# Optimization experiments

Measured on AMD Instinct MI355X. Metric: run time of the kernel, lower is better.

## Reference

```python
import jax, jax.numpy as jnp
import numpy as np

BS, C_IN, S1 = 64, 256, 32
D_OUT, J = 32, 10          # out_dim, num_out_caps (as_final_output -> spatial_size_2)
I = S1 * S1                # num_in_caps = 1024
ROUTE_NUM = 3


def setup_inputs() -> dict:
    key = jax.random.key(0)
    k1, k2, k3 = jax.random.split(key, 3)
    x = jax.random.normal(k1, (BS, C_IN, S1, S1), dtype=jnp.float32)
    W = jax.random.normal(k2, (D_OUT * J, C_IN), dtype=jnp.float32) * 0.02  # 1x1 conv weight
    W_b = jax.random.normal(k3, (D_OUT * J,), dtype=jnp.float32) * 0.02     # conv bias
    return {"x": x, "W": W, "W_b": W_b}


def squash(vec):
    # vec: [bs, j, d]; coeff = ||v||^2 / (1+||v||^2) / ||v||
    norm = jnp.linalg.norm(vec, axis=2, keepdims=True)
    norm_sq = norm * norm
    return vec * (norm_sq / (1.0 + norm_sq) / norm)


def reference(x, W, W_b):
    bs = x.shape[0]
    # 1x1 conv == per-pixel matmul: [bs, J*D, h, w]
    pred = jnp.einsum('bchw,oc->bohw', x, W) + W_b[None, :, None, None]
    # torch: resize(bs, J, D, I) on contiguous tensor, then permute(0,3,1,2)
    pred = pred.reshape(bs, J, D_OUT, I).transpose(0, 3, 1, 2)  # [bs, I, J, D]
    b = jnp.zeros((bs, J, I), dtype=x.dtype)  # b_init='zero'
    v = None
    for _ in range(ROUTE_NUM):
        c = jax.nn.softmax(b, axis=1)                    # softmax over output caps j
        s = jnp.einsum('bji,bijd->bjd', c, pred)          # per-capsule weighted sum
        v = squash(s)                                     # [bs, J, D]
        delta_b = jnp.einsum('bjd,bijd->bji', v, pred)    # agreement
        b = b + jax.lax.stop_gradient(delta_b)            # torch .detach()
    return v  # as_final_output=True -> [bs, J, D]
```

## Files before the change

kernel.cpp:

```cpp
#include <hip/hip_runtime.h>
#include <hip/hip_bf16.h>

typedef __attribute__((ext_vector_type(8))) unsigned short u16x8;
typedef __attribute__((ext_vector_type(4))) unsigned short u16x4;
typedef __attribute__((ext_vector_type(8))) short short8;
typedef __attribute__((ext_vector_type(4))) float floatx4;

#define BS 64
#define CIN 256
#define II 1024
#define OO 320
#define JJ 10
#define DD 32

__device__ __forceinline__ float b2f(unsigned short u) {
    union { unsigned int i; float f; } x; x.i = ((unsigned int)u) << 16; return x.f;
}
__device__ __forceinline__ float b2f_lo(unsigned int v) {
    union { unsigned int i; float f; } x; x.i = v << 16; return x.f;
}
__device__ __forceinline__ float b2f_hi(unsigned int v) {
    union { unsigned int i; float f; } x; x.i = v & 0xffff0000u; return x.f;
}
__device__ __forceinline__ unsigned short f2b(float f) {
    union { float f; unsigned int i; } x; x.f = f;
    unsigned int r = x.i + 0x7fffu + ((x.i >> 16) & 1u);
    return (unsigned short)(r >> 16);
}
__device__ __forceinline__ float redwave(float v) {
    v += __shfl_xor(v, 1);  v += __shfl_xor(v, 2);  v += __shfl_xor(v, 4);
    v += __shfl_xor(v, 8);  v += __shfl_xor(v, 16); v += __shfl_xor(v, 32);
    return v;
}

__global__ __launch_bounds__(256) void k_prepW(const float* __restrict__ W,
                                               unsigned short* __restrict__ Wl) {
    int gid = blockIdx.x * 256 + threadIdx.x;
    int lm = gid & 15;
    int quad = (gid >> 4) & 3;
    int mtl = (gid >> 6) & 3;
    int ks = (gid >> 8) & 7;
    int oc = gid >> 11;
    const float* src = W + (size_t)(oc * 64 + mtl * 16 + lm) * CIN + ks * 32 + quad * 8;
    float4 v0 = *(const float4*)src;
    float4 v1 = *(const float4*)(src + 4);
    u16x8 u;
    u[0] = f2b(v0.x); u[1] = f2b(v0.y); u[2] = f2b(v0.z); u[3] = f2b(v0.w);
    u[4] = f2b(v1.x); u[5] = f2b(v1.y); u[6] = f2b(v1.z); u[7] = f2b(v1.w);
    *(u16x8*)(Wl + (size_t)gid * 8) = u;
}

__global__ __launch_bounds__(512) void k_gemm7(const float* __restrict__ x,
                                               const unsigned short* __restrict__ Wl,
                                               const float* __restrict__ Wb,
                                               unsigned short* __restrict__ pred,
                                               float* __restrict__ psumC) {
    __shared__ unsigned short Bs[128 * 132];
    __shared__ unsigned short AsF[2048 * 8];
    __shared__ float Wb_lds[OO];

    const int ic = blockIdx.x, b = blockIdx.y;
    const int t = threadIdx.x, w = t >> 6, l = t & 63;
    const int lm = l & 15, quad = l >> 4;
    const int i0 = ic * 128;

    if (t < OO) Wb_lds[t] = Wb[t];

    short8 bfrag[8];
    float csum[2];
    const int crow = t >> 5;
    const int f4 = t & 31;
    const int cs_c = t >> 2;
    const int cs_seg = t & 3;
#pragma unroll
    for (int kc = 0; kc < 2; ++kc) {
        float4 fr[8];
#pragma unroll
        for (int p = 0; p < 8; ++p) {
            int c = kc * 128 + p * 16 + crow;
            fr[p] = *(const float4*)(x + ((size_t)b * CIN + c) * II + i0 + 4 * f4);
        }
#pragma unroll
        for (int p = 0; p < 8; ++p) {
            int cl = p * 16 + crow;
            u16x4 u;
            u[0] = f2b(fr[p].x); u[1] = f2b(fr[p].y); u[2] = f2b(fr[p].z); u[3] = f2b(fr[p].w);
            *(u16x4*)&Bs[cl * 132 + 4 * f4] = u;
        }
        __syncthreads();
#pragma unroll
        for (int k2 = 0; k2 < 4; ++k2) {
            short8 f;
#pragma unroll
            for (int j = 0; j < 8; ++j)
                f[j] = (short)Bs[(k2 * 32 + quad * 8 + j) * 132 + w * 16 + lm];
            bfrag[kc * 4 + k2] = f;
        }
        {
            float cs = 0.f;
#pragma unroll
            for (int q = 0; q < 8; ++q) {
                u16x4 u = *(const u16x4*)&Bs[cs_c * 132 + cs_seg * 32 + q * 4];
                cs += b2f(u[0]) + b2f(u[1]) + b2f(u[2]) + b2f(u[3]);
            }
            cs += __shfl_xor(cs, 1);
            cs += __shfl_xor(cs, 2);
            csum[kc] = cs;
        }
        __syncthreads();
    }
    if (cs_seg == 0) {
        size_t cbase = ((size_t)ic * BS + b) * CIN;
        psumC[cbase + cs_c] = csum[0];
        psumC[cbase + 128 + cs_c] = csum[1];
    }

    const int ibase = i0 + w * 16 + lm;
#pragma unroll 1
    for (int oc = 0; oc < 5; ++oc) {
        if (oc > 0) __syncthreads();
        {
            const u16x8* src = (const u16x8*)Wl + oc * 2048;
            u16x8* dst = (u16x8*)AsF;
            for (int u = t; u < 2048; u += 512) dst[u] = src[u];
        }
        __syncthreads();

        floatx4 acc[4] = {};
#pragma unroll
        for (int ks = 0; ks < 8; ++ks)
#pragma unroll
            for (int mtl = 0; mtl < 4; ++mtl) {
                short8 af = *(const short8*)(AsF + (size_t)(((ks * 4 + mtl) * 4 + quad) * 16 + lm) * 8);
                acc[mtl] = __builtin_amdgcn_mfma_f32_16x16x32_bf16(af, bfrag[ks], acc[mtl], 0, 0, 0);
            }

#pragma unroll
        for (int mtl = 0; mtl < 4; ++mtl)
#pragma unroll
            for (int r = 0; r < 4; ++r) {
                int o = oc * 64 + mtl * 16 + quad * 4 + r;
                pred[((size_t)b * OO + o) * II + ibase] = f2b(acc[mtl][r] + Wb_lds[o]);
            }
    }
}

__global__ __launch_bounds__(320) void k_gemv(const float* __restrict__ psumC,
                                              const float* __restrict__ W,
                                              const float* __restrict__ Wb,
                                              float* __restrict__ s1) {
    __shared__ float y_lds[CIN];
    const int b = blockIdx.x, t = threadIdx.x;
    if (t < CIN) {
        float s = 0.f;
#pragma unroll
        for (int sl = 0; sl < 8; ++sl) s += psumC[((size_t)sl * BS + b) * CIN + t];
        y_lds[t] = s;
    }
    __syncthreads();
    const float* wr = W + (size_t)t * CIN;
    float acc = 0.f;
#pragma unroll 4
    for (int c = 0; c < CIN; c += 4) {
        float4 wv = *(const float4*)(wr + c);
        acc += wv.x * y_lds[c] + wv.y * y_lds[c + 1] + wv.z * y_lds[c + 2] + wv.w * y_lds[c + 3];
    }
    s1[(size_t)b * OO + t] = 0.1f * (acc + 1024.0f * Wb[t]);
}

__global__ __launch_bounds__(640) void k_route1(const float* __restrict__ s1,
                                                const unsigned short* __restrict__ pred,
                                                float* __restrict__ blogG,
                                                float* __restrict__ psum1) {
    __shared__ float s_lds[OO];
    __shared__ float v_lds[OO];
    __shared__ float cf[JJ];
    __shared__ float dbuf[JJ][128];

    const int ic = blockIdx.x, b = blockIdx.y;
    const int t = threadIdx.x, w = t >> 6, l = t & 63;

    unsigned int vals[DD];
    {
        const unsigned short* pb = pred + ((size_t)b * OO + w * DD) * II + ic * 128 + 2 * l;
#pragma unroll
        for (int d = 0; d < DD; ++d) vals[d] = *(const unsigned int*)(pb + (size_t)d * II);
    }

    if (t < OO) s_lds[t] = s1[(size_t)b * OO + t];
    __syncthreads();
    if (t < JJ) {
        float n2 = 0.f;
#pragma unroll
        for (int d = 0; d < DD; ++d) { float v = s_lds[t * DD + d]; n2 += v * v; }
        cf[t] = sqrtf(n2) / (1.0f + n2);
    }
    __syncthreads();
    if (t < OO) v_lds[t] = s_lds[t] * cf[t >> 5];
    __syncthreads();

    float d0 = 0.f, d1 = 0.f;
#pragma unroll
    for (int d = 0; d < DD; ++d) {
        float vv = v_lds[w * DD + d];
        d0 += vv * b2f_lo(vals[d]);
        d1 += vv * b2f_hi(vals[d]);
    }
    *(float2*)(blogG + ((size_t)b * JJ + w) * II + ic * 128 + 2 * l) = make_float2(d0, d1);
    dbuf[w][2 * l] = d0; dbuf[w][2 * l + 1] = d1;
    __syncthreads();

    if (t < 128) {
        float lg[JJ];
#pragma unroll
        for (int j = 0; j < JJ; ++j) lg[j] = dbuf[j][t];
        float m = lg[0];
#pragma unroll
        for (int j = 1; j < JJ; ++j) m = fmaxf(m, lg[j]);
        float Z = 0.f, c[JJ];
#pragma unroll
        for (int j = 0; j < JJ; ++j) { c[j] = __expf(lg[j] - m); Z += c[j]; }
        float inv = 1.0f / Z;
#pragma unroll
        for (int j = 0; j < JJ; ++j) dbuf[j][t] = c[j] * inv;
    }
    __syncthreads();

    float c0 = dbuf[w][2 * l], c1 = dbuf[w][2 * l + 1];
#pragma unroll
    for (int d = 0; d < DD; ++d) {
        float p = c0 * b2f_lo(vals[d]) + c1 * b2f_hi(vals[d]);
        p = redwave(p);
        if (l == 0) psum1[((size_t)ic * BS + b) * OO + w * DD + d] = p;
    }
}

__global__ __launch_bounds__(640) void k_route2(const float* __restrict__ psum1,
                                                const unsigned short* __restrict__ pred,
                                                const float* __restrict__ blogG,
                                                float* __restrict__ psum2) {
    __shared__ float s_lds[OO];
    __shared__ float v_lds[OO];
    __shared__ float cf[JJ];
    __shared__ float dbuf[JJ][128];

    const int ic = blockIdx.x, b = blockIdx.y;
    const int t = threadIdx.x, w = t >> 6, l = t & 63;

    unsigned int vals[DD];
    {
        const unsigned short* pb = pred + ((size_t)b * OO + w * DD) * II + ic * 128 + 2 * l;
#pragma unroll
        for (int d = 0; d < DD; ++d) vals[d] = *(const unsigned int*)(pb + (size_t)d * II);
    }

    if (t < OO) {
        float s = 0.f;
#pragma unroll
        for (int sl = 0; sl < 8; ++sl) s += psum1[((size_t)sl * BS + b) * OO + t];
        s_lds[t] = s;
    }
    __syncthreads();
    if (t < JJ) {
        float n2 = 0.f;
#pragma unroll
        for (int d = 0; d < DD; ++d) { float v = s_lds[t * DD + d]; n2 += v * v; }
        cf[t] = sqrtf(n2) / (1.0f + n2);
    }
    __syncthreads();
    if (t < OO) v_lds[t] = s_lds[t] * cf[t >> 5];
    __syncthreads();

    float d0 = 0.f, d1 = 0.f;
#pragma unroll
    for (int d = 0; d < DD; ++d) {
        float vv = v_lds[w * DD + d];
        d0 += vv * b2f_lo(vals[d]);
        d1 += vv * b2f_hi(vals[d]);
    }
    float2 bl = *(const float2*)(blogG + ((size_t)b * JJ + w) * II + ic * 128 + 2 * l);
    dbuf[w][2 * l] = bl.x + d0; dbuf[w][2 * l + 1] = bl.y + d1;
    __syncthreads();

    if (t < 128) {
        float lg[JJ];
#pragma unroll
        for (int j = 0; j < JJ; ++j) lg[j] = dbuf[j][t];
        float m = lg[0];
#pragma unroll
        for (int j = 1; j < JJ; ++j) m = fmaxf(m, lg[j]);
        float Z = 0.f, c[JJ];
#pragma unroll
        for (int j = 0; j < JJ; ++j) { c[j] = __expf(lg[j] - m); Z += c[j]; }
        float inv = 1.0f / Z;
#pragma unroll
        for (int j = 0; j < JJ; ++j) dbuf[j][t] = c[j] * inv;
    }
    __syncthreads();

    float c0 = dbuf[w][2 * l], c1 = dbuf[w][2 * l + 1];
#pragma unroll
    for (int d = 0; d < DD; ++d) {
        float p = c0 * b2f_lo(vals[d]) + c1 * b2f_hi(vals[d]);
        p = redwave(p);
        if (l == 0) psum2[((size_t)ic * BS + b) * OO + w * DD + d] = p;
    }
}

__global__ __launch_bounds__(320) void k_final2(const float* __restrict__ psum2,
                                                float* __restrict__ out) {
    __shared__ float s_lds[OO];
    __shared__ float cf[JJ];
    int b = blockIdx.x, t = threadIdx.x;
    float s = 0.f;
#pragma unroll
    for (int sl = 0; sl < 8; ++sl) s += psum2[((size_t)sl * BS + b) * OO + t];
    s_lds[t] = s;
    __syncthreads();
    if (t < JJ) {
        float n2 = 0.f;
#pragma unroll
        for (int d = 0; d < DD; ++d) { float v = s_lds[t * DD + d]; n2 += v * v; }
        cf[t] = sqrtf(n2) / (1.0f + n2);
    }
    __syncthreads();
    out[b * OO + t] = s_lds[t] * cf[t >> 5];
}

extern "C" void kernel_launch(void* const* d_in, const int* in_sizes, int n_in,
                              void* d_out, int out_size, void* d_ws, size_t ws_size,
                              hipStream_t stream) {
    const float* x  = (const float*)d_in[0];
    const float* W  = (const float*)d_in[1];
    const float* Wb = (const float*)d_in[2];

    char* ws = (char*)d_ws;
    unsigned short* pred = (unsigned short*)ws;
    unsigned short* Wl   = (unsigned short*)(ws + 41943040);
    float* psumC = (float*)(ws + 42106880);
    float* s1    = (float*)(ws + 42631168);
    float* psum1 = (float*)(ws + 42713088);
    float* psum2 = (float*)(ws + 43368448);
    float* blogG = (float*)(ws + 44023808);

    k_prepW<<<40, 256, 0, stream>>>(W, Wl);
    k_gemm7<<<dim3(8, BS), 512, 0, stream>>>(x, Wl, Wb, pred, psumC);
    k_gemv<<<BS, 320, 0, stream>>>(psumC, W, Wb, s1);
    k_route1<<<dim3(8, BS), 640, 0, stream>>>(s1, pred, blogG, psum1);
    k_route2<<<dim3(8, BS), 640, 0, stream>>>(psum1, pred, blogG, psum2);
    k_final2<<<BS, 320, 0, stream>>>(psum2, (float*)d_out);
}
```

Baseline: 171.8 us.

## Transpose pred layout, double-buffer W tiles, and batch wave reductions via butterfly

```diff
diff --git a/kernel.cpp b/kernel.cpp
--- a/kernel.cpp
+++ b/kernel.cpp
@@ -16,21 +16,46 @@
 __device__ __forceinline__ float b2f(unsigned short u) {
     union { unsigned int i; float f; } x; x.i = ((unsigned int)u) << 16; return x.f;
 }
-__device__ __forceinline__ float b2f_lo(unsigned int v) {
-    union { unsigned int i; float f; } x; x.i = v << 16; return x.f;
-}
-__device__ __forceinline__ float b2f_hi(unsigned int v) {
-    union { unsigned int i; float f; } x; x.i = v & 0xffff0000u; return x.f;
-}
 __device__ __forceinline__ unsigned short f2b(float f) {
     union { float f; unsigned int i; } x; x.f = f;
     unsigned int r = x.i + 0x7fffu + ((x.i >> 16) & 1u);
     return (unsigned short)(r >> 16);
 }
-__device__ __forceinline__ float redwave(float v) {
-    v += __shfl_xor(v, 1);  v += __shfl_xor(v, 2);  v += __shfl_xor(v, 4);
-    v += __shfl_xor(v, 8);  v += __shfl_xor(v, 16); v += __shfl_xor(v, 32);
-    return v;
+
+__device__ __forceinline__ float butterfly32(const float* p, int l) {
+    float q16[16];
+#pragma unroll
+    for (int d = 0; d < 16; ++d) {
+        float keep = (l & 1) ? p[2 * d + 1] : p[2 * d];
+        float send = (l & 1) ? p[2 * d] : p[2 * d + 1];
+        q16[d] = keep + __shfl_xor(send, 1);
+    }
+    float q8[8];
+#pragma unroll
+    for (int d = 0; d < 8; ++d) {
+        float keep = (l & 2) ? q16[2 * d + 1] : q16[2 * d];
+        float send = (l & 2) ? q16[2 * d] : q16[2 * d + 1];
+        q8[d] = keep + __shfl_xor(send, 2);
+    }
+    float q4[4];
+#pragma unroll
+    for (int d = 0; d < 4; ++d) {
+        float keep = (l & 4) ? q8[2 * d + 1] : q8[2 * d];
+        float send = (l & 4) ? q8[2 * d] : q8[2 * d + 1];
+        q4[d] = keep + __shfl_xor(send, 4);
+    }
+    float q2[2];
+#pragma unroll
+    for (int d = 0; d < 2; ++d) {
+        float keep = (l & 8) ? q4[2 * d + 1] : q4[2 * d];
+        float send = (l & 8) ? q4[2 * d] : q4[2 * d + 1];
+        q2[d] = keep + __shfl_xor(send, 8);
+    }
+    float keep = (l & 16) ? q2[1] : q2[0];
+    float send = (l & 16) ? q2[0] : q2[1];
+    float q1 = keep + __shfl_xor(send, 16);
+    q1 += __shfl_xor(q1, 32);
+    return q1;
 }
 
 __global__ __launch_bounds__(256) void k_prepW(const float* __restrict__ W,
@@ -50,13 +75,12 @@
     *(u16x8*)(Wl + (size_t)gid * 8) = u;
 }
 
-__global__ __launch_bounds__(512) void k_gemm7(const float* __restrict__ x,
+__global__ __launch_bounds__(512) void k_gemm8(const float* __restrict__ x,
                                                const unsigned short* __restrict__ Wl,
                                                const float* __restrict__ Wb,
                                                unsigned short* __restrict__ pred,
                                                float* __restrict__ psumC) {
-    __shared__ unsigned short Bs[128 * 132];
-    __shared__ unsigned short AsF[2048 * 8];
+    __shared__ unsigned short buf[2][16896];
     __shared__ float Wb_lds[OO];
 
     const int ic = blockIdx.x, b = blockIdx.y;
@@ -66,12 +90,19 @@
 
     if (t < OO) Wb_lds[t] = Wb[t];
 
+    {
+        const u16x8* src = (const u16x8*)Wl;
+        u16x8* dst = (u16x8*)buf[1];
+        dst[t] = src[t];
+        dst[t + 512] = src[t + 512];
+        dst[t + 1024] = src[t + 1024];
+        dst[t + 1536] = src[t + 1536];
+    }
+
     short8 bfrag[8];
     float csum[2];
-    const int crow = t >> 5;
-    const int f4 = t & 31;
-    const int cs_c = t >> 2;
-    const int cs_seg = t & 3;
+    const int crow = t >> 5, f4 = t & 31;
+    const int cs_c = t >> 2, cs_seg = t & 3;
 #pragma unroll
     for (int kc = 0; kc < 2; ++kc) {
         float4 fr[8];
@@ -85,7 +116,7 @@
             int cl = p * 16 + crow;
             u16x4 u;
             u[0] = f2b(fr[p].x); u[1] = f2b(fr[p].y); u[2] = f2b(fr[p].z); u[3] = f2b(fr[p].w);
-            *(u16x4*)&Bs[cl * 132 + 4 * f4] = u;
+            *(u16x4*)&buf[0][cl * 132 + 4 * f4] = u;
         }
         __syncthreads();
 #pragma unroll
@@ -93,14 +124,14 @@
             short8 f;
 #pragma unroll
             for (int j = 0; j < 8; ++j)
-                f[j] = (short)Bs[(k2 * 32 + quad * 8 + j) * 132 + w * 16 + lm];
+                f[j] = (short)buf[0][(k2 * 32 + quad * 8 + j) * 132 + w * 16 + lm];
             bfrag[kc * 4 + k2] = f;
         }
         {
             float cs = 0.f;
 #pragma unroll
             for (int q = 0; q < 8; ++q) {
-                u16x4 u = *(const u16x4*)&Bs[cs_c * 132 + cs_seg * 32 + q * 4];
+                u16x4 u = *(const u16x4*)&buf[0][cs_c * 132 + cs_seg * 32 + q * 4];
                 cs += b2f(u[0]) + b2f(u[1]) + b2f(u[2]) + b2f(u[3]);
             }
             cs += __shfl_xor(cs, 1);
@@ -115,33 +146,35 @@
         psumC[cbase + 128 + cs_c] = csum[1];
     }
 
-    const int ibase = i0 + w * 16 + lm;
+    const size_t predrow = ((size_t)b * II + i0 + w * 16 + lm) * OO;
 #pragma unroll 1
     for (int oc = 0; oc < 5; ++oc) {
-        if (oc > 0) __syncthreads();
-        {
-            const u16x8* src = (const u16x8*)Wl + oc * 2048;
-            u16x8* dst = (u16x8*)AsF;
-            for (int u = t; u < 2048; u += 512) dst[u] = src[u];
-        }
-        __syncthreads();
-
+        if (oc < 4) {
+            const u16x8* src = (const u16x8*)Wl + (size_t)(oc + 1) * 2048;
+            u16x8* dst = (u16x8*)buf[oc & 1];
+            dst[t] = src[t];
+            dst[t + 512] = src[t + 512];
+            dst[t + 1024] = src[t + 1024];
+            dst[t + 1536] = src[t + 1536];
+        }
+        const unsigned short* ab = buf[(oc + 1) & 1];
         floatx4 acc[4] = {};
 #pragma unroll
         for (int ks = 0; ks < 8; ++ks)
 #pragma unroll
             for (int mtl = 0; mtl < 4; ++mtl) {
-                short8 af = *(const short8*)(AsF + (size_t)(((ks * 4 + mtl) * 4 + quad) * 16 + lm) * 8);
+                short8 af = *(const short8*)(ab + (size_t)(((ks * 4 + mtl) * 4 + quad) * 16 + lm) * 8);
                 acc[mtl] = __builtin_amdgcn_mfma_f32_16x16x32_bf16(af, bfrag[ks], acc[mtl], 0, 0, 0);
             }
-
-#pragma unroll
-        for (int mtl = 0; mtl < 4; ++mtl)
-#pragma unroll
-            for (int r = 0; r < 4; ++r) {
-                int o = oc * 64 + mtl * 16 + quad * 4 + r;
-                pred[((size_t)b * OO + o) * II + ibase] = f2b(acc[mtl][r] + Wb_lds[o]);
-            }
+#pragma unroll
+        for (int mtl = 0; mtl < 4; ++mtl) {
+            int ob = oc * 64 + mtl * 16 + quad * 4;
+            u16x4 sv;
+#pragma unroll
+            for (int r = 0; r < 4; ++r) sv[r] = f2b(acc[mtl][r] + Wb_lds[ob + r]);
+            *(u16x4*)(pred + predrow + ob) = sv;
+        }
+        __syncthreads();
     }
 }
 
@@ -180,11 +213,14 @@
     const int ic = blockIdx.x, b = blockIdx.y;
     const int t = threadIdx.x, w = t >> 6, l = t & 63;
 
-    unsigned int vals[DD];
+    u16x8 va[4], vb[4];
     {
-        const unsigned short* pb = pred + ((size_t)b * OO + w * DD) * II + ic * 128 + 2 * l;
-#pragma unroll
-        for (int d = 0; d < DD; ++d) vals[d] = *(const unsigned int*)(pb + (size_t)d * II);
+        const unsigned short* p0 = pred + ((size_t)b * II + ic * 128 + 2 * l) * OO + w * DD;
+#pragma unroll
+        for (int q = 0; q < 4; ++q) {
+            va[q] = *(const u16x8*)(p0 + q * 8);
+            vb[q] = *(const u16x8*)(p0 + OO + q * 8);
+        }
     }
 
     if (t < OO) s_lds[t] = s1[(size_t)b * OO + t];
@@ -201,11 +237,13 @@
 
     float d0 = 0.f, d1 = 0.f;
 #pragma unroll
-    for (int d = 0; d < DD; ++d) {
-        float vv = v_lds[w * DD + d];
-        d0 += vv * b2f_lo(vals[d]);
-        d1 += vv * b2f_hi(vals[d]);
-    }
+    for (int q = 0; q < 4; ++q)
+#pragma unroll
+        for (int e = 0; e < 8; ++e) {
+            float vv = v_lds[w * DD + q * 8 + e];
+            d0 += vv * b2f(va[q][e]);
+            d1 += vv * b2f(vb[q][e]);
+        }
     *(float2*)(blogG + ((size_t)b * JJ + w) * II + ic * 128 + 2 * l) = make_float2(d0, d1);
     dbuf[w][2 * l] = d0; dbuf[w][2 * l + 1] = d1;
     __syncthreads();
@@ -227,12 +265,14 @@
     __syncthreads();
 
     float c0 = dbuf[w][2 * l], c1 = dbuf[w][2 * l + 1];
-#pragma unroll
-    for (int d = 0; d < DD; ++d) {
-        float p = c0 * b2f_lo(vals[d]) + c1 * b2f_hi(vals[d]);
-        p = redwave(p);
-        if (l == 0) psum1[((size_t)ic * BS + b) * OO + w * DD + d] = p;
-    }
+    float p[DD];
+#pragma unroll
+    for (int q = 0; q < 4; ++q)
+#pragma unroll
+        for (int e = 0; e < 8; ++e)
+            p[q * 8 + e] = c0 * b2f(va[q][e]) + c1 * b2f(vb[q][e]);
+    float s = butterfly32(p, l);
+    if (l < 32) psum1[((size_t)ic * BS + b) * OO + w * DD + l] = s;
 }
 
 __global__ __launch_bounds__(640) void k_route2(const float* __restrict__ psum1,
@@ -247,11 +287,14 @@
     const int ic = blockIdx.x, b = blockIdx.y;
     const int t = threadIdx.x, w = t >> 6, l = t & 63;
 
-    unsigned int vals[DD];
+    u16x8 va[4], vb[4];
     {
-        const unsigned short* pb = pred + ((size_t)b * OO + w * DD) * II + ic * 128 + 2 * l;
-#pragma unroll
-        for (int d = 0; d < DD; ++d) vals[d] = *(const unsigned int*)(pb + (size_t)d * II);
+        const unsigned short* p0 = pred + ((size_t)b * II + ic * 128 + 2 * l) * OO + w * DD;
+#pragma unroll
+        for (int q = 0; q < 4; ++q) {
+            va[q] = *(const u16x8*)(p0 + q * 8);
+            vb[q] = *(const u16x8*)(p0 + OO + q * 8);
+        }
     }
 
     if (t < OO) {
@@ -273,11 +316,13 @@
 
     float d0 = 0.f, d1 = 0.f;
 #pragma unroll
-    for (int d = 0; d < DD; ++d) {
-        float vv = v_lds[w * DD + d];
-        d0 += vv * b2f_lo(vals[d]);
-        d1 += vv * b2f_hi(vals[d]);
-    }
+    for (int q = 0; q < 4; ++q)
+#pragma unroll
+        for (int e = 0; e < 8; ++e) {
+            float vv = v_lds[w * DD + q * 8 + e];
+            d0 += vv * b2f(va[q][e]);
+            d1 += vv * b2f(vb[q][e]);
+        }
     float2 bl = *(const float2*)(blogG + ((size_t)b * JJ + w) * II + ic * 128 + 2 * l);
     dbuf[w][2 * l] = bl.x + d0; dbuf[w][2 * l + 1] = bl.y + d1;
     __syncthreads();
@@ -299,12 +344,14 @@
     __syncthreads();
 
     float c0 = dbuf[w][2 * l], c1 = dbuf[w][2 * l + 1];
-#pragma unroll
-    for (int d = 0; d < DD; ++d) {
-        float p = c0 * b2f_lo(vals[d]) + c1 * b2f_hi(vals[d]);
-        p = redwave(p);
-        if (l == 0) psum2[((size_t)ic * BS + b) * OO + w * DD + d] = p;
-    }
+    float p[DD];
+#pragma unroll
+    for (int q = 0; q < 4; ++q)
+#pragma unroll
+        for (int e = 0; e < 8; ++e)
+            p[q * 8 + e] = c0 * b2f(va[q][e]) + c1 * b2f(vb[q][e]);
+    float s = butterfly32(p, l);
+    if (l < 32) psum2[((size_t)ic * BS + b) * OO + w * DD + l] = s;
 }
 
 __global__ __launch_bounds__(320) void k_final2(const float* __restrict__ psum2,
@@ -344,7 +391,7 @@
     float* blogG = (float*)(ws + 44023808);
 
     k_prepW<<<40, 256, 0, stream>>>(W, Wl);
-    k_gemm7<<<dim3(8, BS), 512, 0, stream>>>(x, Wl, Wb, pred, psumC);
+    k_gemm8<<<dim3(8, BS), 512, 0, stream>>>(x, Wl, Wb, pred, psumC);
     k_gemv<<<BS, 320, 0, stream>>>(psumC, W, Wb, s1);
     k_route1<<<dim3(8, BS), 640, 0, stream>>>(s1, pred, blogG, psum1);
     k_route2<<<dim3(8, BS), 640, 0, stream>>>(psum1, pred, blogG, psum2);
```

Result: faster. 153.6 us (-10.6%).
